# Performance work log

Hardware: AMD Instinct MI355X
Metric: run time of the kernel (lower is better)

Reference implementation:

```python
import jax, jax.numpy as jnp
import numpy as np

B, X_DIM, Z_DIM, K = 16384, 784, 64, 64
LOG2PI = 1.8378770664093453


def setup_inputs() -> dict:
    key = jax.random.key(0)
    ks = jax.random.split(key, 8)
    pi_raw = jax.random.uniform(ks[1], (B, K), dtype=jnp.float32) + 1e-3
    pi = pi_raw / jnp.sum(pi_raw, axis=1, keepdims=True)
    return {
        "x": jax.random.normal(ks[0], (B, X_DIM), dtype=jnp.float32),
        "pi": pi,
        "qz_mu": jax.random.normal(ks[2], (B, Z_DIM), dtype=jnp.float32),
        "qz_logsigma": 0.5 * jax.random.normal(ks[3], (B, Z_DIM), dtype=jnp.float32),
        "eps": jax.random.normal(ks[4], (B, Z_DIM), dtype=jnp.float32),
        "pz_y_mu": jax.random.normal(ks[5], (K, Z_DIM), dtype=jnp.float32),
        "pz_y_logsigma": jnp.zeros((K, Z_DIM), dtype=jnp.float32),  # log(init_sigma=1.0)
        "W_dec": jax.random.normal(ks[6], (Z_DIM, X_DIM), dtype=jnp.float32) / np.sqrt(Z_DIM),
        "b_dec": jnp.zeros((X_DIM,), dtype=jnp.float32),
    }


def reference(x, pi, qz_mu, qz_logsigma, eps, pz_y_mu, pz_y_logsigma, W_dec, b_dec):
    # GMMVAE.elbo with num_samples=1; rsample reparameterized with fixed eps.
    qs = jnp.exp(qz_logsigma)                      # [B, z]
    z = qz_mu + qs * eps                           # [B, z]

    # log p(x | z): unit-variance Gaussian likelihood with linear decoder
    mean = z @ W_dec + b_dec                       # [B, x]
    log_px_z = jnp.sum(-0.5 * (x - mean) ** 2 - 0.5 * LOG2PI)

    # py_z: vectorized over all k components (fuses the original Python loop)
    ps = jnp.exp(pz_y_logsigma)                    # [k, z]
    diff = z[:, None, :] - pz_y_mu[None, :, :]     # [B, k, z]
    comp_lp = jnp.sum(-0.5 * (diff / ps[None]) ** 2 - pz_y_logsigma[None] - 0.5 * LOG2PI, axis=-1)  # [B, k]
    log_pi = jnp.log(pi)
    pzy = comp_lp + log_pi                         # [B, k]
    log_py_z = pzy - jax.scipy.special.logsumexp(pzy, axis=1, keepdims=True)
    probs = jnp.exp(log_py_z)                      # [B, k]

    # kl_y = sum_b KL(Cat(py_z) || Cat(pi))
    kl_y = jnp.sum(probs * (log_py_z - log_pi))

    # kl_z = sum_b sum_k probs[b,k] * KL(N(qz_mu, qs) || N(mu_k, ps_k)).sum(z)
    mdiff = qz_mu[:, None, :] - pz_y_mu[None, :, :]  # [B, k, z]
    klz_bk = jnp.sum(
        pz_y_logsigma[None] - qz_logsigma[:, None, :]
        + (qs[:, None, :] ** 2 + mdiff ** 2) / (2.0 * ps[None] ** 2)
        - 0.5,
        axis=-1,
    )                                              # [B, k]
    kl_z = jnp.sum(probs * klz_bk)

    elbo = (log_px_z - kl_y - kl_z) / x.shape[0]
    return elbo
```

## Files before the change

kernel.cpp:

```cpp
#include <hip/hip_runtime.h>

#define NB 16384
#define XD 784
#define ZD 64
#define KK 64
#define LOG2PI_F 1.8378770664093453f

typedef __attribute__((ext_vector_type(8))) short short8;
typedef __attribute__((ext_vector_type(4))) float floatx4;


__device__ __forceinline__ float wave_sum(float x) {
    #pragma unroll
    for (int o = 32; o > 0; o >>= 1) x += __shfl_xor(x, o, 64);
    return x;
}

__device__ __forceinline__ unsigned short f2bf(float f) {
    unsigned u = __float_as_uint(f);
    unsigned r = (u + 0x7FFF + ((u >> 16) & 1)) >> 16;
    return (unsigned short)r;
}

__device__ __forceinline__ unsigned int pack2(float a, float b) {
    return (unsigned int)f2bf(a) | ((unsigned int)f2bf(b) << 16);
}

__device__ __forceinline__ short8 pack8(const float* v) {
    short8 r;
    unsigned int* p = (unsigned int*)&r;
    p[0] = pack2(v[0], v[1]);
    p[1] = pack2(v[2], v[3]);
    p[2] = pack2(v[4], v[5]);
    p[3] = pack2(v[6], v[7]);
    return r;
}

__global__ __launch_bounds__(256) void prep_kernel(
    const float* __restrict__ W, const float* __restrict__ pmu_g,
    const float* __restrict__ plog_g, unsigned short* __restrict__ Wt,
    unsigned short* __restrict__ Bi2, unsigned short* __restrict__ Bm1,
    float* __restrict__ Sk, float* __restrict__ Gk)
{
    const int tid = threadIdx.x;
    if (blockIdx.x < 196) {
        int idx = blockIdx.x * 256 + tid;
        int k = idx / XD;
        int n = idx - k * XD;
        Wt[n * ZD + k] = f2bf(W[idx]);
        return;
    }
    const int k  = tid >> 2;
    const int q  = tid & 3;
    const int v0 = q * 16;
    float s = 0.f, g = 0.f;
    unsigned int* pi2 = (unsigned int*)&Bi2[k * 64 + v0];
    unsigned int* pm1 = (unsigned int*)&Bm1[k * 64 + v0];
    #pragma unroll
    for (int i = 0; i < 4; ++i) {
        float4 mu4 = *(const float4*)&pmu_g[k * 64 + v0 + 4 * i];
        float4 lg4 = *(const float4*)&plog_g[k * 64 + v0 + 4 * i];
        float m0[4] = {mu4.x, mu4.y, mu4.z, mu4.w};
        float l0[4] = {lg4.x, lg4.y, lg4.z, lg4.w};
        float i2v[4], m1v[4];
        #pragma unroll
        for (int j = 0; j < 4; ++j) {
            float i2 = 0.5f * __expf(-2.f * l0[j]);
            i2v[j] = i2;
            m1v[j] = m0[j] * i2;
            g = fmaf(m0[j] * m0[j], i2, g);
            s += l0[j];
        }
        pi2[i * 2 + 0] = pack2(i2v[0], i2v[1]);
        pi2[i * 2 + 1] = pack2(i2v[2], i2v[3]);
        pm1[i * 2 + 0] = pack2(m1v[0], m1v[1]);
        pm1[i * 2 + 1] = pack2(m1v[2], m1v[3]);
    }
    s += __shfl_xor(s, 1, 64);
    s += __shfl_xor(s, 2, 64);
    g += __shfl_xor(g, 1, 64);
    g += __shfl_xor(g, 2, 64);
    if (q == 0) { Sk[k] = s; Gk[k] = g; }
}

__global__ __launch_bounds__(256) void fused_kernel(
    const float* __restrict__ x, const float* __restrict__ pi,
    const float* __restrict__ qmu, const float* __restrict__ qls,
    const float* __restrict__ eps,
    const unsigned short* __restrict__ Bi2, const unsigned short* __restrict__ Bm1,
    const float* __restrict__ Sk, const float* __restrict__ Gk,
    const unsigned short* __restrict__ Wt, const float* __restrict__ bd,
    float* __restrict__ dec_p, float* __restrict__ kly_p, float* __restrict__ klz_p)
{
    const int tid   = threadIdx.x;
    const int lane  = tid & 63;
    const int wid   = tid >> 6;
    const int mm    = lane & 15;
    const int quad  = lane >> 4;
    const int row0  = blockIdx.x * 64;
    const int crow0 = row0 + wid * 16;
    const int arow  = crow0 + mm;
    const int v0    = quad * 8;
    const int v1    = 32 + quad * 8;

    float mu[16], ls[16], ep[16];
    *(float4*)&mu[0]  = *(const float4*)&qmu[arow * 64 + v0];
    *(float4*)&mu[4]  = *(const float4*)&qmu[arow * 64 + v0 + 4];
    *(float4*)&mu[8]  = *(const float4*)&qmu[arow * 64 + v1];
    *(float4*)&mu[12] = *(const float4*)&qmu[arow * 64 + v1 + 4];
    *(float4*)&ls[0]  = *(const float4*)&qls[arow * 64 + v0];
    *(float4*)&ls[4]  = *(const float4*)&qls[arow * 64 + v0 + 4];
    *(float4*)&ls[8]  = *(const float4*)&qls[arow * 64 + v1];
    *(float4*)&ls[12] = *(const float4*)&qls[arow * 64 + v1 + 4];
    *(float4*)&ep[0]  = *(const float4*)&eps[arow * 64 + v0];
    *(float4*)&ep[4]  = *(const float4*)&eps[arow * 64 + v0 + 4];
    *(float4*)&ep[8]  = *(const float4*)&eps[arow * 64 + v1];
    *(float4*)&ep[12] = *(const float4*)&eps[arow * 64 + v1 + 4];

    float zf[16], zz[16], zm[16], q2[16], qm[16];
    float sls = 0.f;
    #pragma unroll
    for (int j = 0; j < 16; ++j) {
        float qs = __expf(ls[j]);
        float z  = fmaf(qs, ep[j], mu[j]);
        zf[j] = z;
        zz[j] = z * z;
        zm[j] = -2.f * z;
        q2[j] = fmaf(mu[j], mu[j], qs * qs);
        qm[j] = -2.f * mu[j];
        sls += ls[j];
    }
    sls += __shfl_xor(sls, 16, 64);
    sls += __shfl_xor(sls, 32, 64);

    const short8 az2_0 = pack8(&zz[0]), az2_1 = pack8(&zz[8]);
    const short8 azm_0 = pack8(&zm[0]), azm_1 = pack8(&zm[8]);
    const short8 aq2_0 = pack8(&q2[0]), aq2_1 = pack8(&q2[8]);
    const short8 aqm_0 = pack8(&qm[0]), aqm_1 = pack8(&qm[8]);
    const short8 af0   = pack8(&zf[0]), af1   = pack8(&zf[8]);

    short8 bi[4][2], bm[4][2];
    float skv[4], gkv[4];
    #pragma unroll
    for (int t = 0; t < 4; ++t) {
        const int kc = t * 16 + mm;
        bi[t][0] = *(const short8*)&Bi2[kc * 64 + v0];
        bi[t][1] = *(const short8*)&Bi2[kc * 64 + v1];
        bm[t][0] = *(const short8*)&Bm1[kc * 64 + v0];
        bm[t][1] = *(const short8*)&Bm1[kc * 64 + v1];
        skv[t] = Sk[kc];
        gkv[t] = Gk[kc];
    }
    float pv[4][4];
    #pragma unroll
    for (int t = 0; t < 4; ++t)
        #pragma unroll
        for (int r = 0; r < 4; ++r)
            pv[t][r] = pi[(crow0 + quad * 4 + r) * 64 + t * 16 + mm];

    floatx4 acc_a[4], acc_c[4];
    #pragma unroll
    for (int t = 0; t < 4; ++t) {
        floatx4 ca = {0.f, 0.f, 0.f, 0.f};
        ca = __builtin_amdgcn_mfma_f32_16x16x32_bf16(az2_0, bi[t][0], ca, 0, 0, 0);
        ca = __builtin_amdgcn_mfma_f32_16x16x32_bf16(az2_1, bi[t][1], ca, 0, 0, 0);
        ca = __builtin_amdgcn_mfma_f32_16x16x32_bf16(azm_0, bm[t][0], ca, 0, 0, 0);
        ca = __builtin_amdgcn_mfma_f32_16x16x32_bf16(azm_1, bm[t][1], ca, 0, 0, 0);
        acc_a[t] = ca;
        floatx4 cc = {0.f, 0.f, 0.f, 0.f};
        cc = __builtin_amdgcn_mfma_f32_16x16x32_bf16(aq2_0, bi[t][0], cc, 0, 0, 0);
        cc = __builtin_amdgcn_mfma_f32_16x16x32_bf16(aq2_1, bi[t][1], cc, 0, 0, 0);
        cc = __builtin_amdgcn_mfma_f32_16x16x32_bf16(aqm_0, bm[t][0], cc, 0, 0, 0);
        cc = __builtin_amdgcn_mfma_f32_16x16x32_bf16(aqm_1, bm[t][1], cc, 0, 0, 0);
        acc_c[t] = cc;
    }

    float comp[4][4], pz[4][4];
    #pragma unroll
    for (int t = 0; t < 4; ++t) {
        const float ck = -skv[t] - 32.0f * LOG2PI_F;
        #pragma unroll
        for (int r = 0; r < 4; ++r) {
            comp[t][r] = ck - (acc_a[t][r] + gkv[t]);
            pz[t][r] = comp[t][r] + __logf(pv[t][r]);
        }
    }

    float kly = 0.f, klz = 0.f;
    #pragma unroll
    for (int r = 0; r < 4; ++r) {
        float mx = fmaxf(fmaxf(pz[0][r], pz[1][r]), fmaxf(pz[2][r], pz[3][r]));
        #pragma unroll
        for (int o = 1; o <= 8; o <<= 1) mx = fmaxf(mx, __shfl_xor(mx, o, 64));
        float e[4];
        float s = 0.f;
        #pragma unroll
        for (int t = 0; t < 4; ++t) { e[t] = __expf(pz[t][r] - mx); s += e[t]; }
        #pragma unroll
        for (int o = 1; o <= 8; o <<= 1) s += __shfl_xor(s, o, 64);
        const float lse = mx + __logf(s);
        const float inv = __frcp_rn(s);
        const float sqr = __shfl(sls, quad * 4 + r, 64);
        #pragma unroll
        for (int t = 0; t < 4; ++t) {
            const float p = e[t] * inv;
            kly = fmaf(p, comp[t][r] - lse, kly);
            klz = fmaf(p, skv[t] - sqr + acc_c[t][r] + gkv[t] - 32.0f, klz);
        }
    }

    kly = wave_sum(kly);
    klz = wave_sum(klz);
    if (lane == 0) {
        kly_p[blockIdx.x * 4 + wid] = kly;
        klz_p[blockIdx.x * 4 + wid] = klz;
    }

    const int xrow = (crow0 + quad * 4) * XD;
    float xa0, xa1, xa2, xa3, bb;
    short8 w0, w1;
    {
        const int col = mm;
        xa0 = x[xrow + 0 * XD + col];
        xa1 = x[xrow + 1 * XD + col];
        xa2 = x[xrow + 2 * XD + col];
        xa3 = x[xrow + 3 * XD + col];
        bb  = bd[col];
        w0  = *(const short8*)&Wt[col * 64 + v0];
        w1  = *(const short8*)&Wt[col * 64 + v1];
    }

    float accl = 0.f;
    #pragma unroll 1
    for (int t = 0; t < 49; ++t) {
        const float cx0 = xa0, cx1 = xa1, cx2 = xa2, cx3 = xa3, cb = bb;
        const short8 cw0 = w0, cw1 = w1;
        if (t + 1 < 49) {
            const int col = (t + 1) * 16 + mm;
            xa0 = x[xrow + 0 * XD + col];
            xa1 = x[xrow + 1 * XD + col];
            xa2 = x[xrow + 2 * XD + col];
            xa3 = x[xrow + 3 * XD + col];
            bb  = bd[col];
            w0  = *(const short8*)&Wt[col * 64 + v0];
            w1  = *(const short8*)&Wt[col * 64 + v1];
        }
        floatx4 c = {0.f, 0.f, 0.f, 0.f};
        c = __builtin_amdgcn_mfma_f32_16x16x32_bf16(af0, cw0, c, 0, 0, 0);
        c = __builtin_amdgcn_mfma_f32_16x16x32_bf16(af1, cw1, c, 0, 0, 0);
        float d0 = cx0 - (c[0] + cb);
        float d1 = cx1 - (c[1] + cb);
        float d2 = cx2 - (c[2] + cb);
        float d3 = cx3 - (c[3] + cb);
        accl = fmaf(d0, d0, accl);
        accl = fmaf(d1, d1, accl);
        accl = fmaf(d2, d2, accl);
        accl = fmaf(d3, d3, accl);
    }

    accl = wave_sum(accl);
    if (lane == 0) dec_p[blockIdx.x * 4 + wid] = -0.5f * accl;
}

__global__ __launch_bounds__(256) void finalize_kernel(
    const float* __restrict__ dec_p, const float* __restrict__ kly_p,
    const float* __restrict__ klz_p, float* __restrict__ out)
{
    __shared__ double s0[256], s1[256], s2[256];
    const int tid = threadIdx.x;
    double a0 = 0.0, a1 = 0.0, a2 = 0.0;
    #pragma unroll
    for (int i = 0; i < 4; ++i) {
        a0 += (double)dec_p[tid + 256 * i];
        a1 += (double)kly_p[tid + 256 * i];
        a2 += (double)klz_p[tid + 256 * i];
    }
    s0[tid] = a0; s1[tid] = a1; s2[tid] = a2;
    __syncthreads();
    #pragma unroll
    for (int off = 128; off > 0; off >>= 1) {
        if (tid < off) {
            s0[tid] += s0[tid + off];
            s1[tid] += s1[tid + off];
            s2[tid] += s2[tid + off];
        }
        __syncthreads();
    }
    if (tid == 0) {
        double lpx = s0[0] - 0.5 * 1.8378770664093453 * (double)NB * (double)XD;
        out[0] = (float)((lpx - s1[0] - s2[0]) / (double)NB);
    }
}

extern "C" void kernel_launch(void* const* d_in, const int* in_sizes, int n_in,
                              void* d_out, int out_size, void* d_ws, size_t ws_size,
                              hipStream_t stream) {
    const float* x    = (const float*)d_in[0];
    const float* pi   = (const float*)d_in[1];
    const float* qmu  = (const float*)d_in[2];
    const float* qls  = (const float*)d_in[3];
    const float* eps  = (const float*)d_in[4];
    const float* pmu  = (const float*)d_in[5];
    const float* plog = (const float*)d_in[6];
    const float* W    = (const float*)d_in[7];
    const float* bd   = (const float*)d_in[8];
    float* out = (float*)d_out;

    char* ws = (char*)d_ws;
    unsigned short* Wt  = (unsigned short*)(ws);
    unsigned short* Bi2 = (unsigned short*)(ws + 100352);
    unsigned short* Bm1 = (unsigned short*)(ws + 108544);
    float* Sk    = (float*)(ws + 116736);
    float* Gk    = (float*)(ws + 116992);
    float* dec_p = (float*)(ws + 117248);
    float* kly_p = (float*)(ws + 121344);
    float* klz_p = (float*)(ws + 125440);

    prep_kernel<<<197, 256, 0, stream>>>(W, pmu, plog, Wt, Bi2, Bm1, Sk, Gk);
    fused_kernel<<<NB / 64, 256, 0, stream>>>(x, pi, qmu, qls, eps,
                                              Bi2, Bm1, Sk, Gk, Wt, bd,
                                              dec_p, kly_p, klz_p);
    finalize_kernel<<<1, 256, 0, stream>>>(dec_p, kly_p, klz_p, out);
}
```

Measured before the change: 137.5 us.

## Split decoder columns across waves and shrink blocks to 16 rows

Each block now covers 16 rows instead of 64, so the grid grows fourfold. The four waves split the 49 decoder column tiles in a stride-4 pattern, and only one wave computes the KL/mixture terms. This targets the low occupancy and latency-bound serial 49-step loop of the old one-block-per-CU launch. In exchange, every wave redundantly loads the qz inputs, the KL wave carries extra work and creates imbalance, and the finalize pass reads four times as many decoder partials.

```diff
diff --git a/kernel.cpp b/kernel.cpp
--- a/kernel.cpp
+++ b/kernel.cpp
@@ -97,9 +97,8 @@
     const int wid   = tid >> 6;
     const int mm    = lane & 15;
     const int quad  = lane >> 4;
-    const int row0  = blockIdx.x * 64;
-    const int crow0 = row0 + wid * 16;
-    const int arow  = crow0 + mm;
+    const int row0  = blockIdx.x * 16;
+    const int arow  = row0 + mm;
     const int v0    = quad * 8;
     const int v1    = 32 + quad * 8;
 
@@ -117,110 +116,117 @@
     *(float4*)&ep[8]  = *(const float4*)&eps[arow * 64 + v1];
     *(float4*)&ep[12] = *(const float4*)&eps[arow * 64 + v1 + 4];
 
-    float zf[16], zz[16], zm[16], q2[16], qm[16];
-    float sls = 0.f;
+    float zf[16], ls_sum = 0.f;
+    float qsv[16];
     #pragma unroll
     for (int j = 0; j < 16; ++j) {
-        float qs = __expf(ls[j]);
-        float z  = fmaf(qs, ep[j], mu[j]);
-        zf[j] = z;
-        zz[j] = z * z;
-        zm[j] = -2.f * z;
-        q2[j] = fmaf(mu[j], mu[j], qs * qs);
-        qm[j] = -2.f * mu[j];
-        sls += ls[j];
-    }
-    sls += __shfl_xor(sls, 16, 64);
-    sls += __shfl_xor(sls, 32, 64);
-
-    const short8 az2_0 = pack8(&zz[0]), az2_1 = pack8(&zz[8]);
-    const short8 azm_0 = pack8(&zm[0]), azm_1 = pack8(&zm[8]);
-    const short8 aq2_0 = pack8(&q2[0]), aq2_1 = pack8(&q2[8]);
-    const short8 aqm_0 = pack8(&qm[0]), aqm_1 = pack8(&qm[8]);
-    const short8 af0   = pack8(&zf[0]), af1   = pack8(&zf[8]);
-
-    short8 bi[4][2], bm[4][2];
-    float skv[4], gkv[4];
-    #pragma unroll
-    for (int t = 0; t < 4; ++t) {
-        const int kc = t * 16 + mm;
-        bi[t][0] = *(const short8*)&Bi2[kc * 64 + v0];
-        bi[t][1] = *(const short8*)&Bi2[kc * 64 + v1];
-        bm[t][0] = *(const short8*)&Bm1[kc * 64 + v0];
-        bm[t][1] = *(const short8*)&Bm1[kc * 64 + v1];
-        skv[t] = Sk[kc];
-        gkv[t] = Gk[kc];
-    }
-    float pv[4][4];
-    #pragma unroll
-    for (int t = 0; t < 4; ++t)
-        #pragma unroll
-        for (int r = 0; r < 4; ++r)
-            pv[t][r] = pi[(crow0 + quad * 4 + r) * 64 + t * 16 + mm];
-
-    floatx4 acc_a[4], acc_c[4];
-    #pragma unroll
-    for (int t = 0; t < 4; ++t) {
-        floatx4 ca = {0.f, 0.f, 0.f, 0.f};
-        ca = __builtin_amdgcn_mfma_f32_16x16x32_bf16(az2_0, bi[t][0], ca, 0, 0, 0);
-        ca = __builtin_amdgcn_mfma_f32_16x16x32_bf16(az2_1, bi[t][1], ca, 0, 0, 0);
-        ca = __builtin_amdgcn_mfma_f32_16x16x32_bf16(azm_0, bm[t][0], ca, 0, 0, 0);
-        ca = __builtin_amdgcn_mfma_f32_16x16x32_bf16(azm_1, bm[t][1], ca, 0, 0, 0);
-        acc_a[t] = ca;
-        floatx4 cc = {0.f, 0.f, 0.f, 0.f};
-        cc = __builtin_amdgcn_mfma_f32_16x16x32_bf16(aq2_0, bi[t][0], cc, 0, 0, 0);
-        cc = __builtin_amdgcn_mfma_f32_16x16x32_bf16(aq2_1, bi[t][1], cc, 0, 0, 0);
-        cc = __builtin_amdgcn_mfma_f32_16x16x32_bf16(aqm_0, bm[t][0], cc, 0, 0, 0);
-        cc = __builtin_amdgcn_mfma_f32_16x16x32_bf16(aqm_1, bm[t][1], cc, 0, 0, 0);
-        acc_c[t] = cc;
-    }
-
-    float comp[4][4], pz[4][4];
-    #pragma unroll
-    for (int t = 0; t < 4; ++t) {
-        const float ck = -skv[t] - 32.0f * LOG2PI_F;
+        qsv[j] = __expf(ls[j]);
+        zf[j]  = fmaf(qsv[j], ep[j], mu[j]);
+        ls_sum += ls[j];
+    }
+    const short8 af0 = pack8(&zf[0]), af1 = pack8(&zf[8]);
+
+    if (wid == 3) {
+        float zz[16], zm[16], q2[16], qm[16];
+        #pragma unroll
+        for (int j = 0; j < 16; ++j) {
+            zz[j] = zf[j] * zf[j];
+            zm[j] = -2.f * zf[j];
+            q2[j] = fmaf(mu[j], mu[j], qsv[j] * qsv[j]);
+            qm[j] = -2.f * mu[j];
+        }
+        float sls = ls_sum;
+        sls += __shfl_xor(sls, 16, 64);
+        sls += __shfl_xor(sls, 32, 64);
+
+        const short8 az2_0 = pack8(&zz[0]), az2_1 = pack8(&zz[8]);
+        const short8 azm_0 = pack8(&zm[0]), azm_1 = pack8(&zm[8]);
+        const short8 aq2_0 = pack8(&q2[0]), aq2_1 = pack8(&q2[8]);
+        const short8 aqm_0 = pack8(&qm[0]), aqm_1 = pack8(&qm[8]);
+
+        short8 bi[4][2], bm[4][2];
+        float skv[4], gkv[4];
+        #pragma unroll
+        for (int t = 0; t < 4; ++t) {
+            const int kc = t * 16 + mm;
+            bi[t][0] = *(const short8*)&Bi2[kc * 64 + v0];
+            bi[t][1] = *(const short8*)&Bi2[kc * 64 + v1];
+            bm[t][0] = *(const short8*)&Bm1[kc * 64 + v0];
+            bm[t][1] = *(const short8*)&Bm1[kc * 64 + v1];
+            skv[t] = Sk[kc];
+            gkv[t] = Gk[kc];
+        }
+        float pv[4][4];
+        #pragma unroll
+        for (int t = 0; t < 4; ++t)
+            #pragma unroll
+            for (int r = 0; r < 4; ++r)
+                pv[t][r] = pi[(row0 + quad * 4 + r) * 64 + t * 16 + mm];
+
+        floatx4 acc_a[4], acc_c[4];
+        #pragma unroll
+        for (int t = 0; t < 4; ++t) {
+            floatx4 ca = {0.f, 0.f, 0.f, 0.f};
+            ca = __builtin_amdgcn_mfma_f32_16x16x32_bf16(az2_0, bi[t][0], ca, 0, 0, 0);
+            ca = __builtin_amdgcn_mfma_f32_16x16x32_bf16(az2_1, bi[t][1], ca, 0, 0, 0);
+            ca = __builtin_amdgcn_mfma_f32_16x16x32_bf16(azm_0, bm[t][0], ca, 0, 0, 0);
+            ca = __builtin_amdgcn_mfma_f32_16x16x32_bf16(azm_1, bm[t][1], ca, 0, 0, 0);
+            acc_a[t] = ca;
+            floatx4 cc = {0.f, 0.f, 0.f, 0.f};
+            cc = __builtin_amdgcn_mfma_f32_16x16x32_bf16(aq2_0, bi[t][0], cc, 0, 0, 0);
+            cc = __builtin_amdgcn_mfma_f32_16x16x32_bf16(aq2_1, bi[t][1], cc, 0, 0, 0);
+            cc = __builtin_amdgcn_mfma_f32_16x16x32_bf16(aqm_0, bm[t][0], cc, 0, 0, 0);
+            cc = __builtin_amdgcn_mfma_f32_16x16x32_bf16(aqm_1, bm[t][1], cc, 0, 0, 0);
+            acc_c[t] = cc;
+        }
+
+        float comp[4][4], pz[4][4];
+        #pragma unroll
+        for (int t = 0; t < 4; ++t) {
+            const float ck = -skv[t] - 32.0f * LOG2PI_F;
+            #pragma unroll
+            for (int r = 0; r < 4; ++r) {
+                comp[t][r] = ck - (acc_a[t][r] + gkv[t]);
+                pz[t][r] = comp[t][r] + __logf(pv[t][r]);
+            }
+        }
+
+        float kly = 0.f, klz = 0.f;
         #pragma unroll
         for (int r = 0; r < 4; ++r) {
-            comp[t][r] = ck - (acc_a[t][r] + gkv[t]);
-            pz[t][r] = comp[t][r] + __logf(pv[t][r]);
-        }
-    }
-
-    float kly = 0.f, klz = 0.f;
-    #pragma unroll
-    for (int r = 0; r < 4; ++r) {
-        float mx = fmaxf(fmaxf(pz[0][r], pz[1][r]), fmaxf(pz[2][r], pz[3][r]));
-        #pragma unroll
-        for (int o = 1; o <= 8; o <<= 1) mx = fmaxf(mx, __shfl_xor(mx, o, 64));
-        float e[4];
-        float s = 0.f;
-        #pragma unroll
-        for (int t = 0; t < 4; ++t) { e[t] = __expf(pz[t][r] - mx); s += e[t]; }
-        #pragma unroll
-        for (int o = 1; o <= 8; o <<= 1) s += __shfl_xor(s, o, 64);
-        const float lse = mx + __logf(s);
-        const float inv = __frcp_rn(s);
-        const float sqr = __shfl(sls, quad * 4 + r, 64);
-        #pragma unroll
-        for (int t = 0; t < 4; ++t) {
-            const float p = e[t] * inv;
-            kly = fmaf(p, comp[t][r] - lse, kly);
-            klz = fmaf(p, skv[t] - sqr + acc_c[t][r] + gkv[t] - 32.0f, klz);
-        }
-    }
-
-    kly = wave_sum(kly);
-    klz = wave_sum(klz);
-    if (lane == 0) {
-        kly_p[blockIdx.x * 4 + wid] = kly;
-        klz_p[blockIdx.x * 4 + wid] = klz;
-    }
-
-    const int xrow = (crow0 + quad * 4) * XD;
+            float mx = fmaxf(fmaxf(pz[0][r], pz[1][r]), fmaxf(pz[2][r], pz[3][r]));
+            #pragma unroll
+            for (int o = 1; o <= 8; o <<= 1) mx = fmaxf(mx, __shfl_xor(mx, o, 64));
+            float e[4];
+            float s = 0.f;
+            #pragma unroll
+            for (int t = 0; t < 4; ++t) { e[t] = __expf(pz[t][r] - mx); s += e[t]; }
+            #pragma unroll
+            for (int o = 1; o <= 8; o <<= 1) s += __shfl_xor(s, o, 64);
+            const float lse = mx + __logf(s);
+            const float inv = __frcp_rn(s);
+            const float sqr = __shfl(sls, quad * 4 + r, 64);
+            #pragma unroll
+            for (int t = 0; t < 4; ++t) {
+                const float p = e[t] * inv;
+                kly = fmaf(p, comp[t][r] - lse, kly);
+                klz = fmaf(p, skv[t] - sqr + acc_c[t][r] + gkv[t] - 32.0f, klz);
+            }
+        }
+
+        kly = wave_sum(kly);
+        klz = wave_sum(klz);
+        if (lane == 0) {
+            kly_p[blockIdx.x] = kly;
+            klz_p[blockIdx.x] = klz;
+        }
+    }
+
+    const int xrow = (row0 + quad * 4) * XD;
     float xa0, xa1, xa2, xa3, bb;
     short8 w0, w1;
     {
-        const int col = mm;
+        const int col = wid * 16 + mm;
         xa0 = x[xrow + 0 * XD + col];
         xa1 = x[xrow + 1 * XD + col];
         xa2 = x[xrow + 2 * XD + col];
@@ -232,11 +238,12 @@
 
     float accl = 0.f;
     #pragma unroll 1
-    for (int t = 0; t < 49; ++t) {
+    for (int t = wid; t < 49; t += 4) {
         const float cx0 = xa0, cx1 = xa1, cx2 = xa2, cx3 = xa3, cb = bb;
         const short8 cw0 = w0, cw1 = w1;
-        if (t + 1 < 49) {
-            const int col = (t + 1) * 16 + mm;
+        const int tn = t + 4;
+        if (tn < 49) {
+            const int col = tn * 16 + mm;
             xa0 = x[xrow + 0 * XD + col];
             xa1 = x[xrow + 1 * XD + col];
             xa2 = x[xrow + 2 * XD + col];
@@ -270,8 +277,9 @@
     const int tid = threadIdx.x;
     double a0 = 0.0, a1 = 0.0, a2 = 0.0;
     #pragma unroll
+    for (int i = 0; i < 16; ++i) a0 += (double)dec_p[tid + 256 * i];
+    #pragma unroll
     for (int i = 0; i < 4; ++i) {
-        a0 += (double)dec_p[tid + 256 * i];
         a1 += (double)kly_p[tid + 256 * i];
         a2 += (double)klz_p[tid + 256 * i];
     }
@@ -313,11 +321,11 @@
     float* Sk    = (float*)(ws + 116736);
     float* Gk    = (float*)(ws + 116992);
     float* dec_p = (float*)(ws + 117248);
-    float* kly_p = (float*)(ws + 121344);
-    float* klz_p = (float*)(ws + 125440);
+    float* kly_p = (float*)(ws + 133632);
+    float* klz_p = (float*)(ws + 137728);
 
     prep_kernel<<<197, 256, 0, stream>>>(W, pmu, plog, Wt, Bi2, Bm1, Sk, Gk);
-    fused_kernel<<<NB / 64, 256, 0, stream>>>(x, pi, qmu, qls, eps,
+    fused_kernel<<<NB / 16, 256, 0, stream>>>(x, pi, qmu, qls, eps,
                                               Bi2, Bm1, Sk, Gk, Wt, bd,
                                               dec_p, kly_p, klz_p);
     finalize_kernel<<<1, 256, 0, stream>>>(dec_p, kly_p, klz_p, out);
```

Result: faster. 129.5 us (-5.8%).
